# Optimization experiments

Measured on AMD Instinct MI355X. Metric: run time of the kernel, lower is better.

Reference implementation:

```python
import jax, jax.numpy as jnp
import numpy as np

FRAME_PERIOD = 80
SAMPLE_RATE = 16000
FFT_LENGTH = 1024
DEFAULT_F0 = 500.0
Q1 = -0.15
F_MIN = 3.0 * SAMPLE_RATE / (FFT_LENGTH - 3)
TAU = 2.0 * np.pi
SAFEGUARD = 1e-12  # noise floor added to windowed waveform
L1 = FFT_LENGTH // 2 + 1  # one-sided spectrum length
RATE = SAMPLE_RATE / FFT_LENGTH  # Hz per FFT bin
PAD = 64  # mirror padding (bins) for linear smoothing; > max half-width 500Hz/(3*RATE)~10.7


def setup_inputs() -> dict:
    key = jax.random.key(0)
    k1, k2 = jax.random.split(key)
    B, T = 8, 160000
    N = T // FRAME_PERIOD + 1  # 2001 frames
    x = jax.random.normal(k1, (B, T), jnp.float32)
    # realistic speech pitch range 100..300 Hz (all > F_MIN=47 Hz)
    f0 = 100.0 + 200.0 * jax.random.uniform(k2, (B, N), jnp.float32)
    return {"x": x, "f0": f0}


def _windowed_waveform(x, f0):
    # x: (B,T), f0: (B,N,1). Pitch-adaptive Hanning window (3 periods), WORLD-style.
    B, T = x.shape
    N = f0.shape[1]
    base = jnp.arange(FFT_LENGTH) - FFT_LENGTH // 2  # (L,)
    half_len = jnp.round(1.5 * SAMPLE_RATE / f0)  # (B,N,1) half window length in samples
    mask = (jnp.abs(base) <= half_len).astype(x.dtype)  # (B,N,L)
    window = (0.5 * jnp.cos(np.pi * (base / (1.5 * SAMPLE_RATE)) * f0) + 0.5) * mask
    centers = jnp.arange(N) * FRAME_PERIOD  # frame centers in samples
    idx = jnp.clip(centers[:, None] + base[None, :], 0, T - 1)  # (N,L)
    seg = x[:, idx]  # (B,N,L)
    noise = jax.random.normal(jax.random.key(1234), (B, N, FFT_LENGTH), x.dtype)
    w = seg * window + noise * SAFEGUARD * mask
    # remove window-weighted mean (zero DC)
    w = w - window * (jnp.sum(w, -1, keepdims=True) / jnp.sum(window, -1, keepdims=True))
    return w


def _dc_correction(ps, f0):
    # add mirrored low-frequency replica below f0 (WORLD DCCorrection)
    k = jnp.arange(L1)
    pos = f0 / RATE - k  # fractional bin of mirror frequency f0 - f, (B,N,L1)
    lo = jnp.clip(jnp.floor(pos).astype(jnp.int32), 0, L1 - 2)
    fr = pos - lo
    rep = (jnp.take_along_axis(ps, lo, -1) * (1.0 - fr)
           + jnp.take_along_axis(ps, lo + 1, -1) * fr)
    return ps + jnp.where(k * RATE < f0, rep, 0.0)


def _linear_smoothing(ps, width):
    # rectangular smoothing of width `width` Hz via cumulative integral (WORLD LinearSmoothing)
    e = jnp.arange(-PAD, L1 + PAD)
    j = jnp.abs(e)
    j = jnp.where(j > L1 - 1, 2 * (L1 - 1) - j, j)  # mirror-reflected bin indices
    ext = ps[..., j]  # (B,N,L1+2*PAD)
    C = jnp.cumsum(ext, -1) * RATE
    C = jnp.concatenate([jnp.zeros(C.shape[:-1] + (1,), C.dtype), C], -1)

    def interp(q):
        lo = jnp.clip(jnp.floor(q).astype(jnp.int32), 0, C.shape[-1] - 2)
        fr = q - lo
        return (jnp.take_along_axis(C, lo, -1) * (1.0 - fr)
                + jnp.take_along_axis(C, lo + 1, -1) * fr)

    k = jnp.arange(L1).astype(ps.dtype)
    hwb = width / (2.0 * RATE)  # half-width in bins, (B,N,1)
    q_hi = k + hwb + PAD + 0.5
    q_lo = k - hwb + PAD + 0.5
    return (interp(q_hi) - interp(q_lo)) / width


def _forward(x, f0):
    f0 = jnp.where(f0 <= F_MIN, DEFAULT_F0, f0)[..., None]  # (B,N,1)
    f0 = jax.lax.stop_gradient(f0)  # original code calls .detach()
    w = _windowed_waveform(x, f0)
    ps = jnp.abs(jnp.fft.rfft(w, n=FFT_LENGTH)) ** 2  # (B,N,L1)
    ps = _dc_correction(ps, f0)
    ps = _linear_smoothing(ps, f0 * (2.0 / 3.0))
    ps = ps + jnp.abs(jax.random.normal(jax.random.key(4321), ps.shape, ps.dtype)) * jnp.finfo(x.dtype).eps
    quefrency = jnp.arange(L1) / SAMPLE_RATE
    z = f0 * quefrency  # (B,N,L1)
    smoothing_lifter = jnp.sinc(z).at[..., 0].set(1.0)
    compensation_lifter = 1.0 - 2.0 * Q1 + 2.0 * Q1 * jnp.cos(TAU * z)
    cepstrum = jnp.fft.irfft(jnp.log(ps).astype(jnp.complex64), n=FFT_LENGTH)[..., :L1]
    lifted = (cepstrum * smoothing_lifter * compensation_lifter).astype(jnp.complex64)
    log_power_spectrum = jnp.fft.hfft(lifted, n=FFT_LENGTH)[..., :L1]
    return log_power_spectrum.astype(x.dtype)


def reference(x, f0):
    return _forward(x, f0)
```

## Files before the change

kernel.cpp:

```cpp
#include <hip/hip_runtime.h>
#include <math.h>

#define PI_F 3.14159265358979323846f

__device__ __forceinline__ void fft512(float2* X, float2* Y, const float2* TW, int t) {
  float2* xr = X; float2* yr = Y;
#pragma unroll
  for (int s = 0; s < 9; ++s) {
    __syncthreads();
    const int m = 1 << s;
    float2 a = xr[t];
    float2 b = xr[t + 256];
    float2 w = TW[t & ~(m - 1)];
    int o = t + (t & ~(m - 1));
    float sr = a.x - b.x, si = a.y - b.y;
    yr[o] = make_float2(a.x + b.x, a.y + b.y);
    yr[o + m] = make_float2(sr * w.x + si * w.y, si * w.x - sr * w.y);
    float2* tp = xr; xr = yr; yr = tp;
  }
  __syncthreads();
}

__device__ __forceinline__ float unpack_re(const float2* Z, const float2* UP, int k) {
  int kk = k & 511, kr = (512 - k) & 511;
  float2 z = Z[kk], u = Z[kr];
  float Er = 0.5f * (z.x + u.x);
  float Or = 0.5f * (z.y + u.y), Oi = 0.5f * (u.x - z.x);
  float2 w = UP[k];
  return Er + w.x * Or + w.y * Oi;
}

__device__ __forceinline__ float unpack_pwr(const float2* Z, const float2* UP, int k) {
  int kk = k & 511, kr = (512 - k) & 511;
  float2 z = Z[kk], u = Z[kr];
  float Er = 0.5f * (z.x + u.x), Ei = 0.5f * (z.y - u.y);
  float Or = 0.5f * (z.y + u.y), Oi = 0.5f * (u.x - z.x);
  float2 w = UP[k];
  float re = Er + w.x * Or + w.y * Oi;
  float im = Ei + w.x * Oi - w.y * Or;
  return re * re + im * im;
}

__global__ __launch_bounds__(256) void init_tables(float2* __restrict__ w2) {
  int i = blockIdx.x * 256 + threadIdx.x;
  if (i < 256) {
    float sn, cs; sincosf((PI_F / 256.0f) * (float)i, &sn, &cs);
    w2[i] = make_float2(cs, sn);
  } else if (i < 769) {
    int k = i - 256;
    float sn, cs; sincosf((PI_F / 512.0f) * (float)k, &sn, &cs);
    w2[i] = make_float2(cs, sn);
  }
}

__global__ __launch_bounds__(256)
void cheaptrick_kernel(const float* __restrict__ x, const float* __restrict__ f0g,
                       float* __restrict__ out, int Tlen, int Nfr,
                       const float2* __restrict__ twg) {
  __shared__ float2 ZA[512], ZB[512];
  __shared__ float2 ps2[257];
  __shared__ float C[642];
  __shared__ float red[16];
  __shared__ float2 TW[256];
  __shared__ float2 UP[513];
  float* ps = (float*)ps2;

  const int t = threadIdx.x;
  const int blk = blockIdx.x;
  const int b = blk / Nfr;
  const int n = blk - b * Nfr;
  const int lane = t & 63, wave = t >> 6;
  const float RATE = 15.625f;

  if (twg) {
    TW[t] = twg[t];
    UP[t] = twg[256 + t];
    UP[t + 257] = twg[256 + t + 257];
    if (t == 0) UP[256] = twg[256 + 256];
  } else {
    float sn, cs;
    sincosf((PI_F / 256.0f) * (float)t, &sn, &cs);
    TW[t] = make_float2(cs, sn);
    sincosf((PI_F / 512.0f) * (float)t, &sn, &cs);
    UP[t] = make_float2(cs, sn);
    sincosf((PI_F / 512.0f) * (float)(t + 257), &sn, &cs);
    UP[t + 257] = make_float2(cs, sn);
    if (t == 0) UP[256] = make_float2(0.0f, 1.0f);
  }

  float f0v = f0g[blk];
  const float F_MIN = 3.0f * 16000.0f / 1021.0f;
  if (f0v <= F_MIN) f0v = 500.0f;

  float half_len = rintf(24000.0f / f0v);
  float wv[4], wd[4];
  float sw = 0.f, swin = 0.f;
  const int center = n * 80;
  const int ids[4] = {2 * t, 2 * t + 1, 2 * t + 512, 2 * t + 513};
#pragma unroll
  for (int q = 0; q < 4; ++q) {
    int base = ids[q] - 512;
    float fb = (float)base;
    float msk = (fabsf(fb) <= half_len) ? 1.0f : 0.0f;
    float win = (0.5f * __cosf(PI_F * (fb / 24000.0f) * f0v) + 0.5f) * msk;
    int src = center + base;
    src = min(max(src, 0), Tlen - 1);
    float wval = x[(size_t)b * (size_t)Tlen + src] * win;
    wd[q] = win; wv[q] = wval;
    sw += wval; swin += win;
  }
#pragma unroll
  for (int off = 32; off > 0; off >>= 1) {
    sw += __shfl_down(sw, off);
    swin += __shfl_down(swin, off);
  }
  if (lane == 0) { red[wave] = sw; red[4 + wave] = swin; }
  __syncthreads();
  float mf = (red[0] + red[1] + red[2] + red[3]) / (red[4] + red[5] + red[6] + red[7]);

  ZA[t]       = make_float2(wv[0] - wd[0] * mf, wv[1] - wd[1] * mf);
  ZA[t + 256] = make_float2(wv[2] - wd[2] * mf, wv[3] - wd[3] * mf);

  fft512(ZA, ZB, TW, t);

  {
    float p0 = unpack_pwr(ZB, UP, t);
    float p1 = unpack_pwr(ZB, UP, t + 256);
    float p2 = (t == 0) ? unpack_pwr(ZB, UP, 512) : 0.f;
    ps[t] = p0; ps[t + 256] = p1;
    if (t == 0) ps[512] = p2;
  }
  __syncthreads();

  {
    float rep = 0.f;
    bool act = (t < 40);
    float kf = (float)t;
    if (act) {
      float pos = f0v / RATE - kf;
      int lo = (int)floorf(pos);
      lo = min(max(lo, 0), 511);
      float fr = pos - (float)lo;
      rep = ps[lo] * (1.0f - fr) + ps[lo + 1] * fr;
    }
    __syncthreads();
    if (act && kf * RATE < f0v) ps[t] += rep;
  }
  __syncthreads();

  {
    const int ebase = 3 * t;
    float e0 = 0.f, e1 = 0.f, e2 = 0.f;
    {
      int e = ebase;
      if (e < 641)     { int j = e - 64;     j = j < 0 ? -j : j; if (j > 512) j = 1024 - j; e0 = ps[j]; }
      if (e + 1 < 641) { int j = e + 1 - 64; j = j < 0 ? -j : j; if (j > 512) j = 1024 - j; e1 = ps[j]; }
      if (e + 2 < 641) { int j = e + 2 - 64; j = j < 0 ? -j : j; if (j > 512) j = 1024 - j; e2 = ps[j]; }
    }
    float psum = e0 + e1 + e2;
    float sc = psum;
#pragma unroll
    for (int off = 1; off < 64; off <<= 1) {
      float v = __shfl_up(sc, off);
      if (lane >= off) sc += v;
    }
    if (lane == 63) red[8 + wave] = sc;
    __syncthreads();
    float woff = 0.f;
#pragma unroll
    for (int w2 = 0; w2 < 4; ++w2) woff += (w2 < wave) ? red[8 + w2] : 0.f;
    float run = woff + (sc - psum);
    if (t == 0) C[0] = 0.f;
    if (ebase < 641)     { run += e0; C[ebase + 1] = RATE * run; }
    if (ebase + 1 < 641) { run += e1; C[ebase + 2] = RATE * run; }
    if (ebase + 2 < 641) { run += e2; C[ebase + 3] = RATE * run; }
  }
  __syncthreads();

  {
    const float width = f0v * (2.0f / 3.0f);
    const float hwb = width * (1.0f / (2.0f * RATE));
    const float winv = 1.0f / width;
    float s0, s1, s2 = 1.f;
#pragma unroll
    for (int r = 0; r < 3; ++r) {
      int k = (r == 0) ? t : (r == 1) ? (t + 256) : 512;
      if (r == 2 && t != 0) break;
      float kf = (float)k;
      float qh = kf + hwb + 64.5f, ql = kf - hwb + 64.5f;
      int lh = (int)floorf(qh); lh = min(max(lh, 0), 640);
      int ll = (int)floorf(ql); ll = min(max(ll, 0), 640);
      float fh = qh - (float)lh, fl = ql - (float)ll;
      float vh = C[lh] * (1.f - fh) + C[lh + 1] * fh;
      float vl = C[ll] * (1.f - fl) + C[ll + 1] * fl;
      float v = (vh - vl) * winv;
      if (r == 0) s0 = v; else if (r == 1) s1 = v; else s2 = v;
    }
    ps[t] = __logf(s0);
    ps[t + 256] = __logf(s1);
    if (t == 0) ps[512] = __logf(s2);
  }
  __syncthreads();

  ZA[t] = ps2[t];
  {
    int idx1 = (2 * t + 512) <= 512 ? (2 * t + 512) : (1024 - (2 * t + 512));
    int idx2 = 1024 - (2 * t + 513);
    ZA[t + 256] = make_float2(ps[idx1], ps[idx2]);
  }
  fft512(ZA, ZB, TW, t);

  {
    const float inv = 1.0f / 1024.0f;
    float l0, l1, l2 = 0.f;
#pragma unroll
    for (int r = 0; r < 3; ++r) {
      int k = (r == 0) ? t : (r == 1) ? (t + 256) : 512;
      if (r == 2 && t != 0) break;
      float cep = unpack_re(ZB, UP, k) * inv;
      float z = f0v * ((float)k * (1.0f / 16000.0f));
      float pz = PI_F * z;
      float s = __sinf(pz);
      float sl = (k == 0) ? 1.0f : (s / pz);
      float cl = 1.0f + 0.6f * s * s;
      float v = cep * sl * cl;
      if (r == 0) l0 = v; else if (r == 1) l1 = v; else l2 = v;
    }
    ps[t] = l0; ps[t + 256] = l1;
    if (t == 0) ps[512] = l2;
  }
  __syncthreads();

  ZA[t] = ps2[t];
  {
    int idx1 = (2 * t + 512) <= 512 ? (2 * t + 512) : (1024 - (2 * t + 512));
    int idx2 = 1024 - (2 * t + 513);
    ZA[t + 256] = make_float2(ps[idx1], ps[idx2]);
  }
  fft512(ZA, ZB, TW, t);

  {
    size_t ob = (size_t)blk * 513;
    out[ob + t]       = unpack_re(ZB, UP, t);
    out[ob + t + 256] = unpack_re(ZB, UP, t + 256);
    if (t == 0) out[ob + 512] = unpack_re(ZB, UP, 512);
  }
}

extern "C" void kernel_launch(void* const* d_in, const int* in_sizes, int n_in,
                              void* d_out, int out_size, void* d_ws, size_t ws_size,
                              hipStream_t stream) {
  (void)n_in; (void)out_size;
  const float* x  = (const float*)d_in[0];
  const float* f0 = (const float*)d_in[1];
  float* out = (float*)d_out;
  int B = in_sizes[1] - in_sizes[0] / 80;
  if (B < 1) B = 1;
  int Tlen = in_sizes[0] / B;
  int Nfr  = in_sizes[1] / B;

  float2* tw = nullptr;
  if (d_ws && ws_size >= 1538 * sizeof(float)) {
    tw = (float2*)d_ws;
    hipLaunchKernelGGL(init_tables, dim3(4), dim3(256), 0, stream, tw);
  }
  hipLaunchKernelGGL(cheaptrick_kernel, dim3(in_sizes[1]), dim3(256), 0, stream,
                     x, f0, out, Tlen, Nfr, (const float2*)tw);
}
```

Baseline: 174.5 us.

## Replace radix-2 shared-memory FFT with radix-4 Stockham stages plus final radix-2

The 512-point complex FFT now uses four radix-4 stages followed by one radix-2 stage, instead of nine radix-2 stages. This cuts the number of block-wide barriers and shared-memory passes in each of the three FFTs per frame. The first radix-4 stage writes 16-byte vector stores, so the shared buffers are aligned to 16 bytes. The trade-off is that only 128 of the 256 threads work in the radix-4 stages, and each of those threads does more arithmetic.

```diff
diff --git a/kernel.cpp b/kernel.cpp
--- a/kernel.cpp
+++ b/kernel.cpp
@@ -3,20 +3,54 @@
 
 #define PI_F 3.14159265358979323846f
 
+__device__ __forceinline__ float2 cmuln(float2 a, float2 w) {
+  return make_float2(a.x * w.x + a.y * w.y, a.y * w.x - a.x * w.y);
+}
+
 __device__ __forceinline__ void fft512(float2* X, float2* Y, const float2* TW, int t) {
   float2* xr = X; float2* yr = Y;
-#pragma unroll
-  for (int s = 0; s < 9; ++s) {
+  __syncthreads();
+  if (t < 128) {
+    float2 a0 = xr[t], a1 = xr[t + 128], a2 = xr[t + 256], a3 = xr[t + 384];
+    float T0x = a0.x + a2.x, T0y = a0.y + a2.y;
+    float T1x = a0.x - a2.x, T1y = a0.y - a2.y;
+    float T2x = a1.x + a3.x, T2y = a1.y + a3.y;
+    float T3x = a1.x - a3.x, T3y = a1.y - a3.y;
+    float4* y4 = (float4*)yr;
+    y4[2 * t]     = make_float4(T0x + T2x, T0y + T2y, T1x + T3y, T1y - T3x);
+    y4[2 * t + 1] = make_float4(T0x - T2x, T0y - T2y, T1x - T3y, T1y + T3x);
+  }
+  { float2* tp = xr; xr = yr; yr = tp; }
+#pragma unroll
+  for (int ns = 4; ns <= 64; ns *= 4) {
     __syncthreads();
-    const int m = 1 << s;
-    float2 a = xr[t];
-    float2 b = xr[t + 256];
-    float2 w = TW[t & ~(m - 1)];
-    int o = t + (t & ~(m - 1));
-    float sr = a.x - b.x, si = a.y - b.y;
-    yr[o] = make_float2(a.x + b.x, a.y + b.y);
-    yr[o + m] = make_float2(sr * w.x + si * w.y, si * w.x - sr * w.y);
-    float2* tp = xr; xr = yr; yr = tp;
+    if (t < 128) {
+      float2 a0 = xr[t], a1 = xr[t + 128], a2 = xr[t + 256], a3 = xr[t + 384];
+      int u = t & (ns - 1);
+      int m1 = u * (128 / ns);
+      float2 w1 = TW[m1], w2 = TW[2 * m1];
+      float2 w3 = make_float2(w1.x * w2.x - w1.y * w2.y, w1.y * w2.x + w1.x * w2.y);
+      float2 b1 = cmuln(a1, w1);
+      float2 b2 = cmuln(a2, w2);
+      float2 b3 = cmuln(a3, w3);
+      float T0x = a0.x + b2.x, T0y = a0.y + b2.y;
+      float T1x = a0.x - b2.x, T1y = a0.y - b2.y;
+      float T2x = b1.x + b3.x, T2y = b1.y + b3.y;
+      float T3x = b1.x - b3.x, T3y = b1.y - b3.y;
+      int idxD = (t / ns) * (4 * ns) + u;
+      yr[idxD]          = make_float2(T0x + T2x, T0y + T2y);
+      yr[idxD + ns]     = make_float2(T1x + T3y, T1y - T3x);
+      yr[idxD + 2 * ns] = make_float2(T0x - T2x, T0y - T2y);
+      yr[idxD + 3 * ns] = make_float2(T1x - T3y, T1y + T3x);
+    }
+    { float2* tp = xr; xr = yr; yr = tp; }
+  }
+  __syncthreads();
+  {
+    float2 a = xr[t], b = xr[t + 256];
+    float2 bw = cmuln(b, TW[t]);
+    yr[t]       = make_float2(a.x + bw.x, a.y + bw.y);
+    yr[t + 256] = make_float2(a.x - bw.x, a.y - bw.y);
   }
   __syncthreads();
 }
@@ -57,7 +91,7 @@
 void cheaptrick_kernel(const float* __restrict__ x, const float* __restrict__ f0g,
                        float* __restrict__ out, int Tlen, int Nfr,
                        const float2* __restrict__ twg) {
-  __shared__ float2 ZA[512], ZB[512];
+  __shared__ __align__(16) float2 ZA[512], ZB[512];
   __shared__ float2 ps2[257];
   __shared__ float C[642];
   __shared__ float red[16];
```

Measured after the change: 156.6 us. -10.3%, faster.
